# Kernel tuning notes

Measured on AMD Instinct MI355X. Metric: run time of the kernel, lower is better.

The kernel has to match this reference:

```python
import jax, jax.numpy as jnp
import numpy as np

B, D, O, I = 64, 128, 512, 512


def setup_inputs() -> dict:
    key = jax.random.key(0)
    k1, k2, k3 = jax.random.split(key, 3)
    inp = jax.random.bernoulli(k1, 0.5, (B, D, I))            # binary activations
    weight_noise = jax.random.bernoulli(k2, 0.5, (D, O, I))   # sigmoid(W) > rand, binary
    # popcount of I fair coins has mean I/2, std sqrt(I)/2; center threshold there
    bias_noise = (I / 2.0 + (jnp.sqrt(I) / 2.0)
                  * jax.random.normal(k3, (D, O), dtype=jnp.float32))
    return {"input": inp, "weight_noise": weight_noise, "bias_noise": bias_noise}


def reference(input, weight_noise, bias_noise):
    # (weight_noise == input).sum(-1) over binary {0,1} tensors equals
    #   dot(w, x) + dot(1-w, 1-x) = I - sum(w) - sum(x) + 2 * dot(w, x)
    # which avoids materializing the (B, D, O, I) comparison tensor.
    x = input.astype(jnp.float32)          # (B, D, I)
    w = weight_noise.astype(jnp.float32)   # (D, O, I)
    dot = jnp.einsum('bdi,doi->bdo', x, w)               # per-direction binary GEMM
    act = (jnp.float32(I) - w.sum(-1)[None, :, :]        # (1, D, O)
           - x.sum(-1)[:, :, None]                        # (B, D, 1)
           + 2.0 * dot)                                   # match counts, (B, D, O)
    return act > bias_noise[None, :, :]                   # bool (B, D, O)
```

## Files before the change

kernel.cpp:

```cpp
#include <hip/hip_runtime.h>
#include <cstdint>

typedef unsigned long long u64;
typedef unsigned int u32;

#define BB 64
#define DD 128
#define OO 512
#define II 512
#define OT 64
#define XROWS (BB * DD)

__device__ __forceinline__ int detect_mode(const u32* __restrict__ w) {
    bool all01 = true, allf = true;
#pragma unroll
    for (int i = 0; i < 32; ++i) {
        u32 v = w[i];
        all01 = all01 && (v <= 1u);
        allf  = allf  && (v == 0u || v == 0x3F800000u);
    }
    return all01 ? 1 : (allf ? 2 : 0);
}

__device__ __forceinline__ u64 ballots8_bytes(u64 v, int lane) {
    u64 keep = 0;
#pragma unroll
    for (int j = 0; j < 8; ++j) {
        u64 bj = __ballot((u32)(v >> (8 * j)) & 1u);
        if (lane == j) keep = bj;
    }
    return keep;
}

__device__ __forceinline__ u64 pack_row(const void* __restrict__ src,
                                        size_t elem0, int mode, int lane) {
    u64 my = 0;
    if (mode == 0) {
        u64 v = *(const u64*)((const uint8_t*)src + elem0 + (size_t)lane * 8);
        my = ballots8_bytes(v, lane);
    } else {
        const u32 sh = (mode == 1) ? 0u : 23u;
        const uint4* p = (const uint4*)((const u32*)src + elem0);
        uint4 a = p[lane];
        uint4 b = p[64 + lane];
        u64 w0 = __ballot((a.x >> sh) & 1u), w1 = __ballot((a.y >> sh) & 1u);
        u64 w2 = __ballot((a.z >> sh) & 1u), w3 = __ballot((a.w >> sh) & 1u);
        u64 w4 = __ballot((b.x >> sh) & 1u), w5 = __ballot((b.y >> sh) & 1u);
        u64 w6 = __ballot((b.z >> sh) & 1u), w7 = __ballot((b.w >> sh) & 1u);
        if (lane == 0) my = w0;  if (lane == 1) my = w1;
        if (lane == 2) my = w2;  if (lane == 3) my = w3;
        if (lane == 4) my = w4;  if (lane == 5) my = w5;
        if (lane == 6) my = w6;  if (lane == 7) my = w7;
    }
    return my;
}

__device__ __forceinline__ void gload_lds16(const void* g, void* lds) {
    __builtin_amdgcn_global_load_lds(
        (const __attribute__((address_space(1))) void*)g,
        (__attribute__((address_space(3))) void*)lds, 16, 0, 0);
}

__global__ __launch_bounds__(256)
void pack_x_kernel(const void* __restrict__ x, const void* __restrict__ w,
                   u64* __restrict__ px) {
    const int gtid = blockIdx.x * 256 + threadIdx.x;
    const int row  = gtid >> 6;
    const int lane = threadIdx.x & 63;
    const int mode = detect_mode((const u32*)w);
    u64 my = pack_row(x, (size_t)row * II, mode, lane);
    if (lane < 8) px[(size_t)row * 8 + lane] = my;
}

__global__ __launch_bounds__(256, 4)
void fused_kernel(const void* __restrict__ x, const void* __restrict__ w,
                  const u64* __restrict__ px,
                  const float* __restrict__ bias, int* __restrict__ out) {
    __shared__ u64 stage64[2048];
    __shared__ u64 wp[OT][9];
    __shared__ u64 xp[BB][8];

    const int tid  = threadIdx.x;
    const int bid  = blockIdx.x;
    const int xcd  = bid & 7;
    const int idx  = bid >> 3;
    const int d    = xcd * 16 + (idx >> 3);
    const int o0   = (idx & 7) * OT;
    const int wv   = tid >> 6;
    const int lane = tid & 63;

    const int mode = detect_mode((const u32*)w);
    const float bv = bias[d * OO + o0 + (tid & 63)];

    uint8_t* stage = (uint8_t*)stage64;

    if (mode == 0) {
        const uint8_t* wtile = (const uint8_t*)w + (size_t)(d * OO + o0) * II;

#pragma unroll
        for (int i = 0; i < 4; ++i) {
            const int inst = wv * 4 + i;
            gload_lds16(wtile + inst * 1024 + lane * 16, stage + inst * 1024);
        }
        {
            const int b = wv * 16 + (lane >> 2);
            gload_lds16((const uint8_t*)px + ((size_t)(b * DD + d)) * 64
                                           + (size_t)(lane & 3) * 16,
                        (uint8_t*)xp + wv * 1024);
        }
        asm volatile("s_waitcnt vmcnt(0)" ::: "memory");
        __syncthreads();

#pragma unroll
        for (int r = 0; r < 8; ++r) {
            const int row = wv * 8 + r;
            u64 v = *(const u64*)(stage + row * 512 + lane * 8);
            u64 k = ballots8_bytes(v, lane);
            if (lane < 8) wp[row][lane] = k;
        }
        __syncthreads();

#pragma unroll
        for (int i = 0; i < 4; ++i) {
            const int inst = wv * 4 + i;
            gload_lds16(wtile + 16384 + inst * 1024 + lane * 16,
                        stage + inst * 1024);
        }
        asm volatile("s_waitcnt vmcnt(0)" ::: "memory");
        __syncthreads();
#pragma unroll
        for (int r = 0; r < 8; ++r) {
            const int row = wv * 8 + r;
            u64 v = *(const u64*)(stage + row * 512 + lane * 8);
            u64 k = ballots8_bytes(v, lane);
            if (lane < 8) wp[32 + row][lane] = k;
        }
        __syncthreads();
    } else {
#pragma unroll
        for (int r = 0; r < 16; ++r) {
            const int o = wv * 16 + r;
            u64 my = pack_row(w, ((size_t)(d * OO + o0 + o)) * II, mode, lane);
            if (lane < 8) wp[o][lane] = my;
        }
        for (int t = tid; t < BB * 8; t += 256) {
            const int b = t >> 3, k = t & 7;
            xp[b][k] = px[((size_t)(b * DD + d)) * 8 + k];
        }
        __syncthreads();
    }

    const int o  = tid & 63;
    const int b0 = (tid >> 6) * 16;

    u64 wr[8];
#pragma unroll
    for (int k = 0; k < 8; ++k) wr[k] = wp[o][k];

    int* outp = out + (size_t)d * OO + o0 + o;
#pragma unroll 4
    for (int bi = 0; bi < 16; ++bi) {
        const int b = b0 + bi;
        int m = 0;
#pragma unroll
        for (int k = 0; k < 8; ++k) m += __popcll(xp[b][k] ^ wr[k]);
        const float act = (float)(512 - m);
        outp[(size_t)b * (DD * OO)] = (act > bv) ? 1 : 0;
    }
}

extern "C" void kernel_launch(void* const* d_in, const int* in_sizes, int n_in,
                              void* d_out, int out_size, void* d_ws, size_t ws_size,
                              hipStream_t stream) {
    const void*  x    = d_in[0];
    const void*  w    = d_in[1];
    const float* bias = (const float*)d_in[2];
    int*         out  = (int*)d_out;
    u64*         px   = (u64*)d_ws;

    pack_x_kernel<<<XROWS / 4, 256, 0, stream>>>(x, w, px);
    fused_kernel<<<DD * (OO / OT), 256, 0, stream>>>(x, w, px, bias, out);
}
```

Measured before the change: 38.62 us.

## Fuse input bit-packing into main kernel and drop separate pack pass

Removes the standalone pack_x kernel and has each block load and bit-pack its own 64 input rows for its direction, alongside staging the full 64-row weight tile into LDS in one pass instead of two halves. This eliminates one kernel launch and the workspace round-trip for packed inputs. In exchange, each input row is now re-read and re-packed by all 8 output-tile blocks sharing a direction, LDS use grows to about 64KB+, and occupancy hint drops from 4 to 2 blocks per CU.

```diff
diff --git a/kernel.cpp b/kernel.cpp
--- a/kernel.cpp
+++ b/kernel.cpp
@@ -9,7 +9,6 @@
 #define OO 512
 #define II 512
 #define OT 64
-#define XROWS (BB * DD)
 
 __device__ __forceinline__ int detect_mode(const u32* __restrict__ w) {
     bool all01 = true, allf = true;
@@ -61,22 +60,11 @@
         (__attribute__((address_space(3))) void*)lds, 16, 0, 0);
 }
 
-__global__ __launch_bounds__(256)
-void pack_x_kernel(const void* __restrict__ x, const void* __restrict__ w,
-                   u64* __restrict__ px) {
-    const int gtid = blockIdx.x * 256 + threadIdx.x;
-    const int row  = gtid >> 6;
-    const int lane = threadIdx.x & 63;
-    const int mode = detect_mode((const u32*)w);
-    u64 my = pack_row(x, (size_t)row * II, mode, lane);
-    if (lane < 8) px[(size_t)row * 8 + lane] = my;
-}
-
-__global__ __launch_bounds__(256, 4)
-void fused_kernel(const void* __restrict__ x, const void* __restrict__ w,
-                  const u64* __restrict__ px,
-                  const float* __restrict__ bias, int* __restrict__ out) {
-    __shared__ u64 stage64[2048];
+__global__ __launch_bounds__(256, 2)
+void binlin_one(const void* __restrict__ x, const void* __restrict__ w,
+                const float* __restrict__ bias, int* __restrict__ out) {
+    __shared__ u64 wstage[4096];
+    __shared__ u64 xstage[4096];
     __shared__ u64 wp[OT][9];
     __shared__ u64 xp[BB][8];
 
@@ -92,48 +80,38 @@
     const int mode = detect_mode((const u32*)w);
     const float bv = bias[d * OO + o0 + (tid & 63)];
 
-    uint8_t* stage = (uint8_t*)stage64;
-
     if (mode == 0) {
         const uint8_t* wtile = (const uint8_t*)w + (size_t)(d * OO + o0) * II;
+        const uint8_t* xb    = (const uint8_t*)x;
 
 #pragma unroll
-        for (int i = 0; i < 4; ++i) {
-            const int inst = wv * 4 + i;
-            gload_lds16(wtile + inst * 1024 + lane * 16, stage + inst * 1024);
+        for (int j = 0; j < 8; ++j) {
+            const int i = wv * 8 + j;
+            gload_lds16(wtile + i * 1024 + lane * 16,
+                        (uint8_t*)wstage + i * 1024 + lane * 16);
         }
-        {
-            const int b = wv * 16 + (lane >> 2);
-            gload_lds16((const uint8_t*)px + ((size_t)(b * DD + d)) * 64
-                                           + (size_t)(lane & 3) * 16,
-                        (uint8_t*)xp + wv * 1024);
-        }
-        asm volatile("s_waitcnt vmcnt(0)" ::: "memory");
-        __syncthreads();
-
 #pragma unroll
-        for (int r = 0; r < 8; ++r) {
-            const int row = wv * 8 + r;
-            u64 v = *(const u64*)(stage + row * 512 + lane * 8);
-            u64 k = ballots8_bytes(v, lane);
-            if (lane < 8) wp[row][lane] = k;
+        for (int j = 0; j < 8; ++j) {
+            const int i = wv * 8 + j;
+            const int b = 2 * i + (lane >> 5);
+            gload_lds16(xb + ((size_t)(b * DD + d)) * II + (size_t)(lane & 31) * 16,
+                        (uint8_t*)xstage + i * 1024 + lane * 16);
         }
         __syncthreads();
 
 #pragma unroll
-        for (int i = 0; i < 4; ++i) {
-            const int inst = wv * 4 + i;
-            gload_lds16(wtile + 16384 + inst * 1024 + lane * 16,
-                        stage + inst * 1024);
+        for (int r = 0; r < 16; ++r) {
+            const int row = wv * 16 + r;
+            u64 v = ((const u64*)wstage)[row * 64 + lane];
+            u64 k = ballots8_bytes(v, lane);
+            if (lane < 8) wp[row][lane] = k;
         }
-        asm volatile("s_waitcnt vmcnt(0)" ::: "memory");
-        __syncthreads();
 #pragma unroll
-        for (int r = 0; r < 8; ++r) {
-            const int row = wv * 8 + r;
-            u64 v = *(const u64*)(stage + row * 512 + lane * 8);
+        for (int r = 0; r < 16; ++r) {
+            const int row = wv * 16 + r;
+            u64 v = ((const u64*)xstage)[row * 64 + lane];
             u64 k = ballots8_bytes(v, lane);
-            if (lane < 8) wp[32 + row][lane] = k;
+            if (lane < 8) xp[row][lane] = k;
         }
         __syncthreads();
     } else {
@@ -143,9 +121,11 @@
             u64 my = pack_row(w, ((size_t)(d * OO + o0 + o)) * II, mode, lane);
             if (lane < 8) wp[o][lane] = my;
         }
-        for (int t = tid; t < BB * 8; t += 256) {
-            const int b = t >> 3, k = t & 7;
-            xp[b][k] = px[((size_t)(b * DD + d)) * 8 + k];
+#pragma unroll
+        for (int r = 0; r < 16; ++r) {
+            const int b = wv * 16 + r;
+            u64 my = pack_row(x, ((size_t)(b * DD + d)) * II, mode, lane);
+            if (lane < 8) xp[b][lane] = my;
         }
         __syncthreads();
     }
@@ -176,8 +156,6 @@
     const void*  w    = d_in[1];
     const float* bias = (const float*)d_in[2];
     int*         out  = (int*)d_out;
-    u64*         px   = (u64*)d_ws;
 
-    pack_x_kernel<<<XROWS / 4, 256, 0, stream>>>(x, w, px);
-    fused_kernel<<<DD * (OO / OT), 256, 0, stream>>>(x, w, px, bias, out);
+    binlin_one<<<DD * (OO / OT), 256, 0, stream>>>(x, w, bias, out);
 }
```

Measured after the change: 45.41 us. +17.6%, slower.
